# Kernel tuning notes

Hardware: AMD Instinct MI355X
Metric: run time of the kernel (lower is better)

## Reference

```python
import jax, jax.numpy as jnp
import numpy as np

A = 200000   # atoms
B = 400000   # directed bonds
H = 300      # hidden_size
AF = 133     # atom_fdim
BF = 147     # bond_fdim
DEPTH = 4    # message passing depth -> DEPTH-1 W_h layers
M = 4096     # molecules in batch


def setup_inputs() -> dict:
    key = jax.random.key(0)
    ks = jax.random.split(key, 10)
    s = 0.05
    f_atoms = jax.random.normal(ks[0], (A, AF), jnp.float32)
    f_bonds = jax.random.normal(ks[1], (B, BF), jnp.float32)
    b_src = jax.random.randint(ks[2], (B,), 0, A, jnp.int32)
    b_dst = jax.random.randint(ks[3], (B,), 0, A, jnp.int32)
    # reverse-bond pairing: bond 2i <-> 2i+1
    b2revb = (jnp.arange(B, dtype=jnp.int32) ^ 1)
    mol_ids = jnp.sort(jax.random.randint(ks[4], (A,), 0, M, jnp.int32))
    W_i_atom = jax.random.normal(ks[5], (AF, H), jnp.float32) * s
    W_i_bond = jax.random.normal(ks[6], (BF, H), jnp.float32) * s
    W_h = jax.random.normal(ks[7], (DEPTH - 1, H, H), jnp.float32) * s
    W_o = jax.random.normal(ks[8], (3 * H, H), jnp.float32) * s
    b_o = jnp.zeros((H,), jnp.float32)
    return dict(f_atoms=f_atoms, f_bonds=f_bonds, W_i_atom=W_i_atom,
                W_i_bond=W_i_bond, W_h=W_h, W_o=W_o, b_o=b_o,
                b_src=b_src, b_dst=b_dst, b2revb=b2revb, mol_ids=mol_ids)


def reference(f_atoms, f_bonds, W_i_atom, W_i_bond, W_h, W_o, b_o,
              b_src, b_dst, b2revb, mol_ids):
    relu = jax.nn.relu
    input_atom = relu(f_atoms @ W_i_atom)   # [A, H]
    input_bond = relu(f_bonds @ W_i_bond)   # [B, H]

    def step(message, Wd):
        # scatter-sum incoming bond messages onto destination atoms
        a_msg = jax.ops.segment_sum(message, b_dst, num_segments=A)  # [A, H]
        # gather back to bonds, subtract reverse-bond message (D-MPNN)
        m = a_msg[b_src] - message[b2revb]                           # [B, H]
        return relu(input_bond + m @ Wd), None

    message, _ = jax.lax.scan(step, input_bond, W_h)  # DEPTH-1 iterations

    a_msg = jax.ops.segment_sum(message, b_dst, num_segments=A)      # [A, H]
    a_input = jnp.concatenate([input_atom, a_msg, input_atom * a_msg], axis=-1)
    atom_h = relu(a_input @ W_o + b_o)                               # [A, H]

    # mean readout per molecule
    sums = jax.ops.segment_sum(atom_h, mol_ids, num_segments=M)      # [M, H]
    counts = jax.ops.segment_sum(jnp.ones((A,), atom_h.dtype), mol_ids, num_segments=M)
    return sums / jnp.clip(counts, 1.0)[:, None]
```

## Files before the change

kernel.cpp:

```cpp
#include <hip/hip_runtime.h>
#include <stdint.h>

#define H   300
#define HP  320
#define CAP 32

using bf8 = __attribute__((ext_vector_type(8))) short;
using s4  = __attribute__((ext_vector_type(4))) short;
using f4  = __attribute__((ext_vector_type(4))) float;

__device__ __forceinline__ float bf2f(unsigned short u){
    union { unsigned int i; float f; } v; v.i = ((unsigned int)u) << 16; return v.f;
}
__device__ __forceinline__ unsigned short f2bf(float x){
    unsigned int u = __builtin_bit_cast(unsigned int, x);
    u = (u + 0x7FFFu + ((u >> 16) & 1u)) >> 16;
    return (unsigned short)u;
}

__global__ void fill_k(const int* __restrict__ b_dst, int* __restrict__ cnt,
                       int* __restrict__ bucket, int nB){
    int e = blockIdx.x * 256 + threadIdx.x;
    if (e >= nB) return;
    int d = b_dst[e];
    int slot = atomicAdd(&cnt[d], 1);
    if (slot < CAP) bucket[(long)d * CAP + slot] = e;
}

__global__ void prep_wt(const float* __restrict__ W, unsigned short* __restrict__ Wt,
                        int Kact, int Kp){
    int idx = blockIdx.x * 256 + threadIdx.x;
    if (idx >= 320 * Kp) return;
    int t  = idx / (320 * 32);
    int r  = idx % (320 * 32);
    int n  = r / 32, kk = r % 32;
    int k  = t * 32 + kk;
    float v = (n < H && k < Kact) ? W[(long)k * H + n] : 0.f;
    Wt[idx] = f2bf(v);
}

__global__ void prep_wto(const float* __restrict__ W, unsigned short* __restrict__ Wt){
    int idx = blockIdx.x * 256 + threadIdx.x;
    if (idx >= 320 * 960) return;
    int t  = idx / (320 * 32);
    int r  = idx % (320 * 32);
    int n  = r / 32, kk = r % 32;
    int k  = t * 32 + kk;
    int sec = k / HP, ksec = k % HP;
    float v = (n < H && ksec < H) ? W[((long)sec * H + ksec) * H + n] : 0.f;
    Wt[idx] = f2bf(v);
}

__global__ __launch_bounds__(256)
void conv_in(const float* __restrict__ X, int rows, int Kact,
             unsigned short* __restrict__ Y){
    int t = blockIdx.x * 256 + threadIdx.x;
    if (t >= rows * 20) return;
    int row = t / 20, c = t % 20;
    int k0 = c * 8;
    bf8 v;
    #pragma unroll
    for (int j = 0; j < 8; j++){
        int k = k0 + j;
        float f = (k < Kact) ? X[(long)row * Kact + k] : 0.f;
        v[j] = (short)f2bf(f);
    }
    *(bf8*)(Y + (long)row * 160 + k0) = v;
}

template<int RL, int BM, int EPI>
__global__ __launch_bounds__(256, 1)
void bstat_k(const unsigned short* __restrict__ A,
             const unsigned short* __restrict__ Wt,
             unsigned short* __restrict__ outb,
             int nTiles)
{
    constexpr int T     = RL / 32;
    constexpr int MF    = BM / 32;
    constexpr int TILEB = BM * RL * 2;

    __shared__ char ldsB[T * 10240];
    __shared__ char ldsA[2][TILEB];

    const int tid  = threadIdx.x;
    const int w    = tid >> 6;
    const int wm   = w >> 1, wn = w & 1;
    const int lane = tid & 63;
    const int lr   = lane & 15;
    const int g    = lane >> 4;
    const int nh   = blockIdx.x & 1;

    for (int idx = tid; idx < T * 640; idx += 256){
        int t  = idx / 640;
        int r  = idx - t * 640;
        int gg = r / 160;
        int n  = r - gg * 160;
        bf8 v = *(const bf8*)(Wt + ((long)t * 320 + nh * 160 + n) * 32 + gg * 8);
        *(bf8*)(ldsB + (long)idx * 16) = v;
    }

    auto dma = [&](int t, int buf){
        const char* g0 = (const char*)A + (long)t * TILEB + tid * 16;
        char* l0 = ldsA[buf] + (w * 64) * 16;
        #pragma unroll
        for (int rd = 0; rd < 5; rd++)
            __builtin_amdgcn_global_load_lds(
                (const __attribute__((address_space(1))) void*)(g0 + rd * 4096),
                (__attribute__((address_space(3))) void*)(l0 + rd * 4096),
                16, 0, 0);
    };

    int tile = blockIdx.x >> 1;
    if (tile < nTiles) dma(tile, 0);
    __syncthreads();

    int buf = 0;
    for (; tile < nTiles; tile += 128){
        int nt = tile + 128;
        if (nt < nTiles) dma(nt, buf ^ 1);

        f4 acc[MF][5];
        #pragma unroll
        for (int mf = 0; mf < MF; mf++)
            #pragma unroll
            for (int nf = 0; nf < 5; nf++)
                acc[mf][nf] = (f4){0.f, 0.f, 0.f, 0.f};

        #pragma unroll
        for (int t = 0; t < T; t++){
            bf8 bfr[5], af[MF];
            const char* bb = ldsB + (((t * 4 + g) * 160) + wn * 80 + lr) * 16;
            #pragma unroll
            for (int nf = 0; nf < 5; nf++)
                bfr[nf] = *(const bf8*)(bb + nf * 256);
            #pragma unroll
            for (int mf = 0; mf < MF; mf++){
                int row = wm * (BM / 2) + mf * 16 + lr;
                af[mf] = *(const bf8*)(ldsA[buf] + row * (RL * 2) + (t * 4 + g) * 16);
            }
            #pragma unroll
            for (int mf = 0; mf < MF; mf++)
                #pragma unroll
                for (int nf = 0; nf < 5; nf++)
                    acc[mf][nf] = __builtin_amdgcn_mfma_f32_16x16x32_bf16(
                        bfr[nf], af[mf], acc[mf][nf], 0, 0, 0);
        }

        #pragma unroll
        for (int mf = 0; mf < MF; mf++){
            const long row = (long)tile * BM + wm * (BM / 2) + mf * 16 + lr;
            #pragma unroll
            for (int nf = 0; nf < 5; nf++){
                const int colg = nh * 160 + wn * 80 + nf * 16 + g * 4;
                s4 v4;
                #pragma unroll
                for (int q = 0; q < 4; q++){
                    float v = acc[mf][nf][q];
                    if constexpr (EPI == 0) v = fmaxf(v, 0.f);
                    v4[q] = (short)f2bf(v);
                }
                *(s4*)(outb + row * HP + colg) = v4;
            }
        }
        __syncthreads();
        buf ^= 1;
    }
}

__global__ __launch_bounds__(256, 4)
void gemm_wo(const unsigned short* __restrict__ A0,
             const unsigned short* __restrict__ A1,
             const unsigned short* __restrict__ A2,
             const unsigned short* __restrict__ Wt,
             const float* __restrict__ b_o,
             unsigned short* __restrict__ outb,
             int nTiles)
{
    constexpr int KS = 10;

    __shared__ char lds[32 * 640];

    const int tid  = threadIdx.x;
    const int w    = tid >> 6;
    const int lane = tid & 63;
    const int lr   = lane & 15;
    const int g    = lane >> 4;

    int tile = blockIdx.x;
    if (tile >= nTiles) return;
    const long rowBase = (long)tile * 32;

    const unsigned short* Ap[3] = {A0, A1, A2};

    auto stageA = [&](int sec){
        const char* gb = (const char*)(Ap[sec] + rowBase * HP);
        bf8 st[5];
        #pragma unroll
        for (int i = 0; i < 5; i++)
            st[i] = *(const bf8*)(gb + (i * 256 + tid) * 16);
        #pragma unroll
        for (int i = 0; i < 5; i++){
            int f = i * 256 + tid;
            int row = f / 40, c = f % 40;
            *(bf8*)(lds + row * 640 + ((c ^ (row & 7)) << 4)) = st[i];
        }
    };

    bf8 bb[2][5];
    auto loadB = [&](int t, bf8 (&dst)[5]){
        const unsigned short* base = Wt + ((long)t * 320) * 32 + g * 8;
        #pragma unroll
        for (int n = 0; n < 5; n++)
            dst[n] = *(const bf8*)(base + (w * 80 + n * 16 + lr) * 32);
    };

    f4 acc[2][5];
    #pragma unroll
    for (int m = 0; m < 2; m++)
        #pragma unroll
        for (int n = 0; n < 5; n++)
            acc[m][n] = (f4){0.f, 0.f, 0.f, 0.f};

    #pragma unroll
    for (int sec = 0; sec < 3; ++sec){
        if (sec > 0) __syncthreads();
        stageA(sec);
        loadB(sec * KS + 0, bb[0]);
        __syncthreads();
        loadB(sec * KS + 1, bb[1]);

        #pragma unroll
        for (int i = 0; i < KS; i++){
            bf8 af[2];
            #pragma unroll
            for (int m = 0; m < 2; m++){
                int row = m * 16 + lr;
                int ch  = i * 4 + g;
                af[m] = *(const bf8*)(lds + row * 640 + ((ch ^ (row & 7)) << 4));
            }
            #pragma unroll
            for (int m = 0; m < 2; m++)
                #pragma unroll
                for (int n = 0; n < 5; n++)
                    acc[m][n] = __builtin_amdgcn_mfma_f32_16x16x32_bf16(
                        bb[i & 1][n], af[m], acc[m][n], 0, 0, 0);
            if (i + 2 < KS) loadB(sec * KS + i + 2, bb[i & 1]);
        }
    }

    #pragma unroll
    for (int m = 0; m < 2; m++){
        const long row = rowBase + m * 16 + lr;
        #pragma unroll
        for (int n = 0; n < 5; n++){
            const int colg = w * 80 + n * 16 + g * 4;
            s4 v4;
            #pragma unroll
            for (int q = 0; q < 4; q++){
                int col = colg + q;
                float v = acc[m][n][q];
                v += (col < H ? b_o[col] : 0.f);
                v4[q] = (short)f2bf(fmaxf(v, 0.f));
            }
            *(s4*)(outb + row * HP + colg) = v4;
        }
    }
}

__global__ __launch_bounds__(256)
void comb_k(const unsigned short* __restrict__ MW,
            const unsigned short* __restrict__ bond_in,
            const int* __restrict__ b_src, const int* __restrict__ b2revb,
            const int* __restrict__ cnt, const int* __restrict__ bucket,
            unsigned short* __restrict__ out, int nB){
    int t = blockIdx.x * 256 + threadIdx.x;
    if (t >= nB * 40) return;
    int e = t / 40, ch = t % 40;
    int k0 = ch * 8;
    int s   = b_src[e];
    int rev = b2revb[e];
    int dg = cnt[s]; if (dg > CAP) dg = CAP;
    long base = (long)s * CAP;
    int be0 = 0, be1 = 0, be2 = 0, be3 = 0;
    if (dg > 0) be0 = bucket[base + 0];
    if (dg > 1) be1 = bucket[base + 1];
    if (dg > 2) be2 = bucket[base + 2];
    if (dg > 3) be3 = bucket[base + 3];
    bf8 bi = *(const bf8*)(bond_in + (long)e * HP + k0);
    bf8 rv = *(const bf8*)(MW + (long)rev * HP + k0);
    bf8 m0, m1, m2, m3;
    if (dg > 0) m0 = *(const bf8*)(MW + (long)be0 * HP + k0);
    if (dg > 1) m1 = *(const bf8*)(MW + (long)be1 * HP + k0);
    if (dg > 2) m2 = *(const bf8*)(MW + (long)be2 * HP + k0);
    if (dg > 3) m3 = *(const bf8*)(MW + (long)be3 * HP + k0);
    float sacc[8];
    #pragma unroll
    for (int q = 0; q < 8; q++)
        sacc[q] = bf2f((unsigned short)bi[q]) - bf2f((unsigned short)rv[q]);
    auto addv = [&](bf8 mm){
        #pragma unroll
        for (int q = 0; q < 8; q++) sacc[q] += bf2f((unsigned short)mm[q]);
    };
    if (dg > 0) addv(m0);
    if (dg > 1) addv(m1);
    if (dg > 2) addv(m2);
    if (dg > 3) addv(m3);
    for (int j = 4; j < dg; ++j){
        int be = bucket[base + j];
        addv(*(const bf8*)(MW + (long)be * HP + k0));
    }
    bf8 v;
    #pragma unroll
    for (int q = 0; q < 8; q++) v[q] = (short)f2bf(fmaxf(sacc[q], 0.f));
    *(bf8*)(out + (long)e * HP + k0) = v;
}

__global__ __launch_bounds__(256)
void amsg_k(const unsigned short* __restrict__ msg, const int* __restrict__ cnt,
            const int* __restrict__ bucket,
            const unsigned short* __restrict__ input_atom,
            unsigned short* __restrict__ amsg, unsigned short* __restrict__ prod,
            int nA){
    int t = blockIdx.x * 256 + threadIdx.x;
    if (t >= nA * 40) return;
    int a = t / 40, ch = t % 40;
    int k0 = ch * 8;
    int dg = cnt[a]; if (dg > CAP) dg = CAP;
    long base = (long)a * CAP;
    int be0 = 0, be1 = 0, be2 = 0, be3 = 0;
    if (dg > 0) be0 = bucket[base + 0];
    if (dg > 1) be1 = bucket[base + 1];
    if (dg > 2) be2 = bucket[base + 2];
    if (dg > 3) be3 = bucket[base + 3];
    bf8 ia = *(const bf8*)(input_atom + (long)a * HP + k0);
    bf8 m0, m1, m2, m3;
    if (dg > 0) m0 = *(const bf8*)(msg + (long)be0 * HP + k0);
    if (dg > 1) m1 = *(const bf8*)(msg + (long)be1 * HP + k0);
    if (dg > 2) m2 = *(const bf8*)(msg + (long)be2 * HP + k0);
    if (dg > 3) m3 = *(const bf8*)(msg + (long)be3 * HP + k0);
    float s[8];
    #pragma unroll
    for (int q = 0; q < 8; q++) s[q] = 0.f;
    auto addv = [&](bf8 mm){
        #pragma unroll
        for (int q = 0; q < 8; q++) s[q] += bf2f((unsigned short)mm[q]);
    };
    if (dg > 0) addv(m0);
    if (dg > 1) addv(m1);
    if (dg > 2) addv(m2);
    if (dg > 3) addv(m3);
    for (int j = 4; j < dg; ++j)
        addv(*(const bf8*)(msg + (long)bucket[base + j] * HP + k0));
    bf8 va, vp;
    #pragma unroll
    for (int q = 0; q < 8; q++){
        va[q] = (short)f2bf(s[q]);
        vp[q] = (short)f2bf(s[q] * bf2f((unsigned short)ia[q]));
    }
    *(bf8*)(amsg + (long)a * HP + k0) = va;
    *(bf8*)(prod + (long)a * HP + k0) = vp;
}

__global__ __launch_bounds__(320)
void readout_k(const unsigned short* __restrict__ atom_h,
               const int* __restrict__ mol_ids, int nAtoms,
               float* __restrict__ out){
    int m = blockIdx.x;
    int t = threadIdx.x;
    int lo = 0, hi = nAtoms;
    while (lo < hi){ int mid = (lo + hi) >> 1; if (mol_ids[mid] < m) lo = mid + 1; else hi = mid; }
    int lo2 = lo, hi2 = nAtoms;
    while (lo2 < hi2){ int mid = (lo2 + hi2) >> 1; if (mol_ids[mid] < m + 1) lo2 = mid + 1; else hi2 = mid; }
    if (t < H){
        float s = 0.f;
        for (int a = lo; a < lo2; ++a) s += bf2f(atom_h[(long)a * HP + t]);
        int c2 = lo2 - lo;
        out[(long)m * H + t] = s / (float)(c2 > 0 ? c2 : 1);
    }
}

extern "C" void kernel_launch(void* const* d_in, const int* in_sizes, int n_in,
                              void* d_out, int out_size, void* d_ws, size_t ws_size,
                              hipStream_t stream){
    const float* f_atoms  = (const float*)d_in[0];
    const float* f_bonds  = (const float*)d_in[1];
    const float* W_i_atom = (const float*)d_in[2];
    const float* W_i_bond = (const float*)d_in[3];
    const float* W_h      = (const float*)d_in[4];
    const float* W_o      = (const float*)d_in[5];
    const float* b_o      = (const float*)d_in[6];
    const int* b_src   = (const int*)d_in[7];
    const int* b_dst   = (const int*)d_in[8];
    const int* b2revb  = (const int*)d_in[9];
    const int* mol_ids = (const int*)d_in[10];

    const int nA = in_sizes[10];
    const int nB = in_sizes[7];
    const int nM = out_size / H;

    char* p = (char*)d_ws;
    auto alloc = [&](size_t bytes){ char* q = p; p += (bytes + 255) & ~(size_t)255; return q; };
    unsigned short* Wt_ia = (unsigned short*)alloc((size_t)320 * 160 * 2);
    unsigned short* Wt_ib = (unsigned short*)alloc((size_t)320 * 160 * 2);
    unsigned short* Wt_h  = (unsigned short*)alloc((size_t)3 * 320 * 320 * 2);
    unsigned short* Wt_o  = (unsigned short*)alloc((size_t)320 * 960 * 2);
    int* cnt    = (int*)alloc((size_t)nA * 4);
    int* bucket = (int*)alloc((size_t)nA * CAP * 4);
    unsigned short* input_atom = (unsigned short*)alloc((size_t)nA * HP * 2);
    unsigned short* input_bond = (unsigned short*)alloc((size_t)nB * HP * 2);
    unsigned short* msgA = (unsigned short*)alloc((size_t)nB * HP * 2);
    unsigned short* MW   = (unsigned short*)alloc((size_t)nB * HP * 2);
    unsigned short* fa_bf  = MW;
    unsigned short* fb_bf  = MW + (size_t)nA * 160;
    unsigned short* amsg   = MW;
    unsigned short* prod   = MW + (size_t)nA * HP;
    unsigned short* atom_h = input_bond;

    if ((size_t)(p - (char*)d_ws) > ws_size) return;

    hipMemsetAsync(cnt, 0, (size_t)nA * 4, stream);
    fill_k<<<dim3((nB + 255) / 256), dim3(256), 0, stream>>>(b_dst, cnt, bucket, nB);

    prep_wt<<<dim3((320*160 + 255)/256), dim3(256), 0, stream>>>(W_i_atom, Wt_ia, 133, 160);
    prep_wt<<<dim3((320*160 + 255)/256), dim3(256), 0, stream>>>(W_i_bond, Wt_ib, 147, 160);
    for (int d = 0; d < 3; d++)
        prep_wt<<<dim3((320*320 + 255)/256), dim3(256), 0, stream>>>(
            W_h + (size_t)d * H * H, Wt_h + (size_t)d * 320 * 320, 300, 320);
    prep_wto<<<dim3((320*960 + 255)/256), dim3(256), 0, stream>>>(W_o, Wt_o);
    conv_in<<<dim3((nA*20 + 255)/256), dim3(256), 0, stream>>>(f_atoms, nA, 133, fa_bf);
    conv_in<<<dim3((nB*20 + 255)/256), dim3(256), 0, stream>>>(f_bonds, nB, 147, fb_bf);

    bstat_k<160,64,0><<<dim3(256), dim3(256), 0, stream>>>(
        fa_bf, Wt_ia, input_atom, nA / 64);
    bstat_k<160,64,0><<<dim3(256), dim3(256), 0, stream>>>(
        fb_bf, Wt_ib, input_bond, nB / 64);

    const int combGrid = (nB * 40 + 255) / 256;
    const unsigned short* msg_cur = input_bond;
    for (int d = 0; d < 3; d++){
        bstat_k<320,32,1><<<dim3(256), dim3(256), 0, stream>>>(
            msg_cur, Wt_h + (size_t)d * 320 * 320, MW, nB / 32);
        comb_k<<<dim3(combGrid), dim3(256), 0, stream>>>(
            MW, input_bond, b_src, b2revb, cnt, bucket, msgA, nB);
        msg_cur = msgA;
    }

    amsg_k<<<dim3((nA * 40 + 255) / 256), dim3(256), 0, stream>>>(
        msgA, cnt, bucket, input_atom, amsg, prod, nA);

    gemm_wo<<<dim3(nA / 32), dim3(256), 0, stream>>>(
        input_atom, amsg, prod, Wt_o, b_o, atom_h, nA / 32);

    readout_k<<<dim3(nM), dim3(320), 0, stream>>>(atom_h, mol_ids, nA, (float*)d_out);
}
```

Baseline: 2.166 ms.

## Fuse atom-message product into output GEMM and stage A tiles via direct LDS loads

The input_atom*a_msg product is no longer computed and stored by amsg_k. gemm_wo now builds it on the fly from two LDS-resident tiles, which removes one [A,300] bf16 write and its later read. Both A tiles are loaded once with global_load_lds straight into unswizzled LDS, and the three K sections become one 30-step loop. LDS per block grows to 40KB and the unswizzled layout may cause bank conflicts, which could limit occupancy at 4 blocks per CU.

```diff
diff --git a/kernel.cpp b/kernel.cpp
--- a/kernel.cpp
+++ b/kernel.cpp
@@ -170,15 +170,13 @@
 __global__ __launch_bounds__(256, 4)
 void gemm_wo(const unsigned short* __restrict__ A0,
              const unsigned short* __restrict__ A1,
-             const unsigned short* __restrict__ A2,
              const unsigned short* __restrict__ Wt,
              const float* __restrict__ b_o,
              unsigned short* __restrict__ outb,
              int nTiles)
 {
-    constexpr int KS = 10;
-
-    __shared__ char lds[32 * 640];
+    __shared__ char lds0[20480];
+    __shared__ char lds1[20480];
 
     const int tid  = threadIdx.x;
     const int w    = tid >> 6;
@@ -190,21 +188,24 @@
     if (tile >= nTiles) return;
     const long rowBase = (long)tile * 32;
 
-    const unsigned short* Ap[3] = {A0, A1, A2};
-
-    auto stageA = [&](int sec){
-        const char* gb = (const char*)(Ap[sec] + rowBase * HP);
-        bf8 st[5];
-        #pragma unroll
-        for (int i = 0; i < 5; i++)
-            st[i] = *(const bf8*)(gb + (i * 256 + tid) * 16);
-        #pragma unroll
-        for (int i = 0; i < 5; i++){
-            int f = i * 256 + tid;
-            int row = f / 40, c = f % 40;
-            *(bf8*)(lds + row * 640 + ((c ^ (row & 7)) << 4)) = st[i];
+    {
+        const char* g0 = (const char*)(A0 + rowBase * HP) + tid * 16;
+        const char* g1 = (const char*)(A1 + rowBase * HP) + tid * 16;
+        char* l0 = lds0 + (w * 64) * 16;
+        char* l1 = lds1 + (w * 64) * 16;
+        #pragma unroll
+        for (int rd = 0; rd < 5; rd++){
+            __builtin_amdgcn_global_load_lds(
+                (const __attribute__((address_space(1))) void*)(g0 + rd * 4096),
+                (__attribute__((address_space(3))) void*)(l0 + rd * 4096),
+                16, 0, 0);
+            __builtin_amdgcn_global_load_lds(
+                (const __attribute__((address_space(1))) void*)(g1 + rd * 4096),
+                (__attribute__((address_space(3))) void*)(l1 + rd * 4096),
+                16, 0, 0);
         }
-    };
+    }
+    __syncthreads();
 
     bf8 bb[2][5];
     auto loadB = [&](int t, bf8 (&dst)[5]){
@@ -221,31 +222,36 @@
         for (int n = 0; n < 5; n++)
             acc[m][n] = (f4){0.f, 0.f, 0.f, 0.f};
 
-    #pragma unroll
-    for (int sec = 0; sec < 3; ++sec){
-        if (sec > 0) __syncthreads();
-        stageA(sec);
-        loadB(sec * KS + 0, bb[0]);
-        __syncthreads();
-        loadB(sec * KS + 1, bb[1]);
-
-        #pragma unroll
-        for (int i = 0; i < KS; i++){
-            bf8 af[2];
-            #pragma unroll
-            for (int m = 0; m < 2; m++){
-                int row = m * 16 + lr;
-                int ch  = i * 4 + g;
-                af[m] = *(const bf8*)(lds + row * 640 + ((ch ^ (row & 7)) << 4));
+    loadB(0, bb[0]);
+    loadB(1, bb[1]);
+
+    #pragma unroll
+    for (int t = 0; t < 30; t++){
+        const int tt = t % 10;
+        bf8 af[2];
+        #pragma unroll
+        for (int m = 0; m < 2; m++){
+            const int off = (m * 16 + lr) * 640 + (tt * 4 + g) * 16;
+            if (t < 10){
+                af[m] = *(const bf8*)(lds0 + off);
+            } else if (t < 20){
+                af[m] = *(const bf8*)(lds1 + off);
+            } else {
+                bf8 a = *(const bf8*)(lds0 + off);
+                bf8 b = *(const bf8*)(lds1 + off);
+                #pragma unroll
+                for (int q = 0; q < 8; q++)
+                    af[m][q] = (short)f2bf(bf2f((unsigned short)a[q]) *
+                                           bf2f((unsigned short)b[q]));
             }
-            #pragma unroll
-            for (int m = 0; m < 2; m++)
-                #pragma unroll
-                for (int n = 0; n < 5; n++)
-                    acc[m][n] = __builtin_amdgcn_mfma_f32_16x16x32_bf16(
-                        bb[i & 1][n], af[m], acc[m][n], 0, 0, 0);
-            if (i + 2 < KS) loadB(sec * KS + i + 2, bb[i & 1]);
         }
+        #pragma unroll
+        for (int m = 0; m < 2; m++)
+            #pragma unroll
+            for (int n = 0; n < 5; n++)
+                acc[m][n] = __builtin_amdgcn_mfma_f32_16x16x32_bf16(
+                    bb[t & 1][n], af[m], acc[m][n], 0, 0, 0);
+        if (t + 2 < 30) loadB(t + 2, bb[t & 1]);
     }
 
     #pragma unroll
@@ -318,9 +324,7 @@
 __global__ __launch_bounds__(256)
 void amsg_k(const unsigned short* __restrict__ msg, const int* __restrict__ cnt,
             const int* __restrict__ bucket,
-            const unsigned short* __restrict__ input_atom,
-            unsigned short* __restrict__ amsg, unsigned short* __restrict__ prod,
-            int nA){
+            unsigned short* __restrict__ amsg, int nA){
     int t = blockIdx.x * 256 + threadIdx.x;
     if (t >= nA * 40) return;
     int a = t / 40, ch = t % 40;
@@ -332,7 +336,6 @@
     if (dg > 1) be1 = bucket[base + 1];
     if (dg > 2) be2 = bucket[base + 2];
     if (dg > 3) be3 = bucket[base + 3];
-    bf8 ia = *(const bf8*)(input_atom + (long)a * HP + k0);
     bf8 m0, m1, m2, m3;
     if (dg > 0) m0 = *(const bf8*)(msg + (long)be0 * HP + k0);
     if (dg > 1) m1 = *(const bf8*)(msg + (long)be1 * HP + k0);
@@ -351,14 +354,10 @@
     if (dg > 3) addv(m3);
     for (int j = 4; j < dg; ++j)
         addv(*(const bf8*)(msg + (long)bucket[base + j] * HP + k0));
-    bf8 va, vp;
-    #pragma unroll
-    for (int q = 0; q < 8; q++){
-        va[q] = (short)f2bf(s[q]);
-        vp[q] = (short)f2bf(s[q] * bf2f((unsigned short)ia[q]));
-    }
+    bf8 va;
+    #pragma unroll
+    for (int q = 0; q < 8; q++) va[q] = (short)f2bf(s[q]);
     *(bf8*)(amsg + (long)a * HP + k0) = va;
-    *(bf8*)(prod + (long)a * HP + k0) = vp;
 }
 
 __global__ __launch_bounds__(320)
@@ -413,7 +412,6 @@
     unsigned short* fa_bf  = MW;
     unsigned short* fb_bf  = MW + (size_t)nA * 160;
     unsigned short* amsg   = MW;
-    unsigned short* prod   = MW + (size_t)nA * HP;
     unsigned short* atom_h = input_bond;
 
     if ((size_t)(p - (char*)d_ws) > ws_size) return;
@@ -446,10 +444,10 @@
     }
 
     amsg_k<<<dim3((nA * 40 + 255) / 256), dim3(256), 0, stream>>>(
-        msgA, cnt, bucket, input_atom, amsg, prod, nA);
+        msgA, cnt, bucket, amsg, nA);
 
     gemm_wo<<<dim3(nA / 32), dim3(256), 0, stream>>>(
-        input_atom, amsg, prod, Wt_o, b_o, atom_h, nA / 32);
+        input_atom, amsg, Wt_o, b_o, atom_h, nA / 32);
 
     readout_k<<<dim3(nM), dim3(320), 0, stream>>>(atom_h, mol_ids, nA, (float*)d_out);
 }
```

Result: slower. 2.359 ms (+8.9%).
